# Optimization experiments

Hardware: AMD Instinct MI355X
Metric: run time of the kernel (lower is better)

The kernel has to match this reference:

```python
import jax, jax.numpy as jnp
import numpy as np

B, T, HOP = 4, 200, 120
N = T * HOP
M1, A1 = 40, 5            # mcep_order+1, apdc_order+1
HID, COND = 256, 192
SR = 24000.0
ALPHA = 0.466             # frequency-warping for 24 kHz
PD = 4                    # Pade order
PADE = jnp.asarray([1.0, 0.4999273, 0.1067005, 0.00956526, 0.0003041358], jnp.float32)
SIGN = jnp.asarray([1.0, -1.0, 1.0, -1.0], jnp.float32)  # + for odd Pade tap index
F0_MEAN, F0_STD = 5.0, 0.25
MCEP_MEAN, MCEP_STD = 0.0, 1.0
APDC_MEAN, APDC_STD = 0.0, 1.0
NOISE_RATIO, SP_RATE, F0_RATE = 0.5, 1.0, 1.0


def mc2b(mc, a):
    """SPTK mc2b: mel-cepstrum -> MLSA filter coefficients (scan over order)."""
    mc_rev = jnp.moveaxis(mc, -1, 0)[::-1]  # [M1, B, T]
    def step(carry, c):
        b = c - a * carry
        return b, b
    _, bs = jax.lax.scan(step, jnp.zeros_like(mc_rev[0]), mc_rev)
    return jnp.moveaxis(bs[::-1], 0, -1)


def _mlsafir(x, b, d):
    # SPTK mlsafir, vectorized over the PD Pade taps.
    # x: [PD], b: [M1], d: [PD, M1+1]
    aa = 1.0 - ALPHA * ALPHA
    d1 = aa * x + ALPHA * d[:, 1]
    def step(prev, di):  # d_new[i] = d[i] + a*(d[i+1] - d_new[i-1]) : order recurrence
        d_i, d_ip1 = di
        new = d_i + ALPHA * (d_ip1 - prev)
        return new, new
    xs = (d[:, 2:M1].T, d[:, 3:M1 + 1].T)  # [M1-2, PD]
    _, dupd = jax.lax.scan(step, d1, xs)    # [M1-2, PD]
    y = jnp.einsum('mp,m->p', dupd, b[2:])
    # delay-line shift: new d = [x, d1, d1, dupd[2..M]]
    new_d = jnp.concatenate([x[:, None], d1[:, None], d1[:, None], dupd.T], axis=1)
    return y, new_d


def _mlsa_step(state, inp):
    d1a, d1b, d2, pt2 = state
    x, b = inp
    x = x * jnp.exp(b[0])           # gain
    # ---- stage 1 (uses b[1] only), SPTK mlsadf1 ----
    aa = 1.0 - ALPHA * ALPHA
    na = aa * d1b[:PD] + ALPHA * d1a[1:]
    npt = na * b[1]
    v1 = npt * PADE[1:]
    x1 = x + jnp.sum(v1 * SIGN)
    y1 = jnp.sum(v1) + x1
    d1a = jnp.concatenate([d1a[:1], na])
    d1b = jnp.concatenate([x1[None], npt])
    # ---- stage 2 (orders >= 2), SPTK mlsadf2 ----
    fy, d2 = _mlsafir(pt2[:PD], b, d2)
    v2 = fy * PADE[1:]
    x2 = y1 + jnp.sum(v2 * SIGN)
    y2 = jnp.sum(v2) + x2
    pt2 = jnp.concatenate([x2[None], fy])
    return (d1a, d1b, d2, pt2), y2


def mlsa_filter(exc, b_up):
    # exc: [N], b_up: [N, M1] -> filtered waveform [N]
    init = (jnp.zeros(PD + 1, jnp.float32), jnp.zeros(PD + 1, jnp.float32),
            jnp.zeros((PD, M1 + 1), jnp.float32), jnp.zeros(PD + 1, jnp.float32))
    _, y = jax.lax.scan(_mlsa_step, init, (exc, b_up))
    return y


def _forward(mceps, apdcs, frame_f0s, noise,
             Wm, bm, Wa, ba, Wf, bf, Wpa, bpa, Wpp, bpp,
             Wrp, brp, Wra, bra, Wap):
    # linear feature embed + sum
    hs = mceps @ Wm + bm + apdcs @ Wa + ba + frame_f0s @ Wf + bf   # [B,T,HID]
    ca = hs @ Wpa + bpa                                             # prenet_a cond [B,T,COND]
    cp = hs @ Wpp + bpp                                             # prenet_p cond
    # denorm (+ exp for log-f0)
    f0 = jnp.exp(frame_f0s[..., 0] * F0_STD + F0_MEAN) * F0_RATE    # [B,T]
    sp = mceps * MCEP_STD + MCEP_MEAN
    ap = apdcs * APDC_STD + APDC_MEAN
    # per-path mel-cepstra with prenet residuals
    mc_p = sp * SP_RATE + 0.1 * jnp.tanh(cp @ Wrp + brp)
    mc_a = sp * SP_RATE + 0.1 * jnp.tanh(ca @ Wra + bra) + ap @ Wap
    b_p = mc2b(mc_p, ALPHA)
    b_a = mc2b(mc_a, ALPHA)
    # excitation at sample rate
    f0_up = jnp.repeat(f0, HOP, axis=1)                             # [B,N]
    phase = jnp.cumsum(f0_up / SR, axis=1)
    w = jnp.floor(phase)
    wprev = jnp.concatenate([jnp.zeros_like(w[:, :1]), w[:, :-1]], axis=1)
    amp = jnp.sqrt(SR / jnp.maximum(f0_up, 1.0))
    pulse = jnp.where(w > wprev, amp, 0.0)
    exc_p = pulse * (1.0 - NOISE_RATIO)
    exc_a = noise * NOISE_RATIO
    # run both (periodic/aperiodic) MLSA synthesis filters in one batched scan
    excs = jnp.concatenate([exc_p, exc_a], axis=0)                  # [2B,N]
    bs = jnp.repeat(jnp.concatenate([b_p, b_a], axis=0), HOP, axis=1)  # [2B,N,M1]
    wavs = jax.vmap(mlsa_filter)(excs, bs)                          # [2B,N]
    return wavs[:B] + wavs[B:]


_forward_jit = jax.jit(_forward)


def setup_inputs() -> dict:
    key = jax.random.key(0)
    ks = jax.random.split(key, 20)
    decay = 0.3 / (1.0 + jnp.arange(M1, dtype=jnp.float32))  # realistic cepstral decay (filter stability)
    return {
        'mceps': jax.random.normal(ks[0], (B, T, M1), jnp.float32) * decay,
        'apdcs': jax.random.normal(ks[1], (B, T, A1), jnp.float32) * 0.3,
        'frame_f0s': jax.random.normal(ks[2], (B, T, 1), jnp.float32),
        'noise': jax.random.normal(ks[3], (B, N), jnp.float32),
        'Wm': jax.random.normal(ks[4], (M1, HID), jnp.float32) / np.sqrt(M1),
        'bm': jnp.zeros((HID,), jnp.float32),
        'Wa': jax.random.normal(ks[5], (A1, HID), jnp.float32) / np.sqrt(A1),
        'ba': jnp.zeros((HID,), jnp.float32),
        'Wf': jax.random.normal(ks[6], (1, HID), jnp.float32),
        'bf': jnp.zeros((HID,), jnp.float32),
        'Wpa': jax.random.normal(ks[7], (HID, COND), jnp.float32) / np.sqrt(HID),
        'bpa': jnp.zeros((COND,), jnp.float32),
        'Wpp': jax.random.normal(ks[8], (HID, COND), jnp.float32) / np.sqrt(HID),
        'bpp': jnp.zeros((COND,), jnp.float32),
        'Wrp': jax.random.normal(ks[9], (COND, M1), jnp.float32) / np.sqrt(COND),
        'brp': jnp.zeros((M1,), jnp.float32),
        'Wra': jax.random.normal(ks[10], (COND, M1), jnp.float32) / np.sqrt(COND),
        'bra': jnp.zeros((M1,), jnp.float32),
        'Wap': jax.random.normal(ks[11], (A1, M1), jnp.float32) * 0.05,
    }


def reference(mceps, apdcs, frame_f0s, noise,
              Wm, bm, Wa, ba, Wf, bf, Wpa, bpa, Wpp, bpp,
              Wrp, brp, Wra, bra, Wap):
    return _forward_jit(mceps, apdcs, frame_f0s, noise,
                        Wm, bm, Wa, ba, Wf, bf, Wpa, bpa, Wpp, bpp,
                        Wrp, brp, Wra, bra, Wap)
```

## Files before the change

### kernel.cpp

```cpp
#include <hip/hip_runtime.h>
#include <math.h>

#define ALPHA 0.466f
#define T_FRAMES 200
#define HOPW 120
#define NSAMP 24000
#define M1 40
#define HID 256
#define CONDW 192

#define NCHUNK 100
#define CHUNKF 2
#define WARMF 4
#define SERF (WARMF + CHUNKF)

#define F8 8
#define BPF ((NSAMP + 255) / 256)

__global__ __launch_bounds__(256) void embed_kernel(
    const float* __restrict__ mceps, const float* __restrict__ apdcs,
    const float* __restrict__ f0s,
    const float* __restrict__ Wm, const float* __restrict__ bm,
    const float* __restrict__ Wa, const float* __restrict__ ba,
    const float* __restrict__ Wf, const float* __restrict__ bf,
    const float* __restrict__ Wpa, const float* __restrict__ bpa,
    const float* __restrict__ Wpp, const float* __restrict__ bpp,
    const float* __restrict__ Wrp, const float* __restrict__ brp,
    const float* __restrict__ Wra, const float* __restrict__ bra,
    const float* __restrict__ Wap, float* __restrict__ bcoef)
{
    __shared__ float s_mc[F8][M1];
    __shared__ float s_ap[F8][5];
    __shared__ float s_f0[F8];
    __shared__ float s_h[F8][HID];
    __shared__ float s_ca[F8][CONDW];
    __shared__ float s_cp[F8][CONDW];
    __shared__ float s_mcp[F8][M1];
    __shared__ float s_mca[F8][M1];

    const int tid = threadIdx.x;
    const int R0 = blockIdx.x * F8;

    for (int j = tid; j < F8 * M1; j += 256) s_mc[j / M1][j % M1] = mceps[R0 * M1 + j];
    if (tid < F8 * 5) s_ap[tid / 5][tid % 5] = apdcs[R0 * 5 + tid];
    if (tid < F8)     s_f0[tid] = f0s[R0 + tid];
    __syncthreads();

    {
        float acc[F8];
        const float bias = bm[tid] + ba[tid] + bf[tid];
        #pragma unroll
        for (int r = 0; r < F8; ++r) acc[r] = bias;
        for (int k = 0; k < M1; ++k) {
            float w = Wm[k * HID + tid];
            #pragma unroll
            for (int r = 0; r < F8; ++r) acc[r] = fmaf(s_mc[r][k], w, acc[r]);
        }
        #pragma unroll
        for (int k = 0; k < 5; ++k) {
            float w = Wa[k * HID + tid];
            #pragma unroll
            for (int r = 0; r < F8; ++r) acc[r] = fmaf(s_ap[r][k], w, acc[r]);
        }
        float wf = Wf[tid];
        #pragma unroll
        for (int r = 0; r < F8; ++r) s_h[r][tid] = fmaf(s_f0[r], wf, acc[r]);
    }
    __syncthreads();

    if (tid < CONDW) {
        float aA[F8], aP[F8];
        #pragma unroll
        for (int r = 0; r < F8; ++r) { aA[r] = bpa[tid]; aP[r] = bpp[tid]; }
        for (int k = 0; k < HID; k += 4) {
            float4 h4[F8];
            #pragma unroll
            for (int r = 0; r < F8; ++r) h4[r] = *(const float4*)&s_h[r][k];
            #pragma unroll
            for (int kk = 0; kk < 4; ++kk) {
                float wa = Wpa[(k + kk) * CONDW + tid];
                float wp = Wpp[(k + kk) * CONDW + tid];
                #pragma unroll
                for (int r = 0; r < F8; ++r) {
                    float hv = (&h4[r].x)[kk];
                    aA[r] = fmaf(hv, wa, aA[r]);
                    aP[r] = fmaf(hv, wp, aP[r]);
                }
            }
        }
        #pragma unroll
        for (int r = 0; r < F8; ++r) { s_ca[r][tid] = aA[r]; s_cp[r][tid] = aP[r]; }
    }
    __syncthreads();

    if (tid < M1) {
        const int u = tid;
        float acc[F8];
        #pragma unroll
        for (int r = 0; r < F8; ++r) acc[r] = brp[u];
        for (int k = 0; k < CONDW; k += 4) {
            float4 c4[F8];
            #pragma unroll
            for (int r = 0; r < F8; ++r) c4[r] = *(const float4*)&s_cp[r][k];
            #pragma unroll
            for (int kk = 0; kk < 4; ++kk) {
                float w = Wrp[(k + kk) * M1 + u];
                #pragma unroll
                for (int r = 0; r < F8; ++r) acc[r] = fmaf((&c4[r].x)[kk], w, acc[r]);
            }
        }
        #pragma unroll
        for (int r = 0; r < F8; ++r)
            s_mcp[r][u] = s_mc[r][u] + 0.1f * tanhf(acc[r]);
    } else if (tid >= 64 && tid < 64 + M1) {
        const int u = tid - 64;
        float acc[F8];
        #pragma unroll
        for (int r = 0; r < F8; ++r) acc[r] = bra[u];
        for (int k = 0; k < CONDW; k += 4) {
            float4 c4[F8];
            #pragma unroll
            for (int r = 0; r < F8; ++r) c4[r] = *(const float4*)&s_ca[r][k];
            #pragma unroll
            for (int kk = 0; kk < 4; ++kk) {
                float w = Wra[(k + kk) * M1 + u];
                #pragma unroll
                for (int r = 0; r < F8; ++r) acc[r] = fmaf((&c4[r].x)[kk], w, acc[r]);
            }
        }
        #pragma unroll
        for (int r = 0; r < F8; ++r) {
            float aw = 0.f;
            #pragma unroll
            for (int j = 0; j < 5; ++j) aw = fmaf(s_ap[r][j], Wap[j * M1 + u], aw);
            s_mca[r][u] = s_mc[r][u] + 0.1f * tanhf(acc[r]) + aw;
        }
    }
    __syncthreads();

    if (tid < 16) {
        const int r = tid >> 1, path = tid & 1;
        const int R = R0 + r;
        const int batch = R / T_FRAMES, t = R - batch * T_FRAMES;
        const float* src = path ? s_mca[r] : s_mcp[r];
        float* dst = bcoef + ((path * 4 + batch) * T_FRAMES + t) * M1;
        float prev = src[M1 - 1];
        dst[M1 - 1] = prev;
        for (int m = M1 - 2; m >= 0; --m) {
            prev = src[m] - ALPHA * prev;
            dst[m] = prev;
        }
    }
}

__global__ __launch_bounds__(256) void exc_kernel(
    const float* __restrict__ f0s, const float* __restrict__ noise,
    float* __restrict__ exc)
{
    const int ff = blockIdx.x / BPF;
    const int n = (blockIdx.x % BPF) * 256 + threadIdx.x;
    const int tid = threadIdx.x;

    if (ff >= 4) {
        if (n < NSAMP) exc[ff * NSAMP + n] = 0.5f * noise[(ff - 4) * NSAMP + n];
        return;
    }

    __shared__ double s_base[T_FRAMES];
    __shared__ double s_step[T_FRAMES];
    __shared__ float  s_amp[T_FRAMES];

    if (tid < 64) {
        const int L = tid;
        double st[4], loc[4];
        float am[4];
        double s = 0.0;
        #pragma unroll
        for (int j = 0; j < 4; ++j) {
            int ft = L * 4 + j;
            if (ft < T_FRAMES) {
                double fv = exp((double)f0s[ff * T_FRAMES + ft] * 0.25 + 5.0);
                st[j] = fv / 24000.0;
                am[j] = (float)(0.5 * sqrt(24000.0 / fmax(fv, 1.0)));
            } else { st[j] = 0.0; am[j] = 0.f; }
            loc[j] = s;
            s += st[j];
        }
        double tot = s;
        #pragma unroll
        for (int off = 1; off < 64; off <<= 1) {
            double v = __shfl_up(s, off, 64);
            if (L >= off) s += v;
        }
        double excl = s - tot;
        #pragma unroll
        for (int j = 0; j < 4; ++j) {
            int ft = L * 4 + j;
            if (ft < T_FRAMES) {
                s_base[ft] = 120.0 * (excl + loc[j]);
                s_step[ft] = st[j];
                s_amp[ft]  = am[j];
            }
        }
    }
    __syncthreads();

    if (n < NSAMP) {
        int ft = n / HOPW, k = n - ft * HOPW;
        double st = s_step[ft], bs = s_base[ft];
        double ph  = bs + (double)(k + 1) * st;
        double php = bs + (double)k * st;
        exc[ff * NSAMP + n] = (floor(ph) > floor(php)) ? s_amp[ft] : 0.0f;
    }
}

template <int CTRL>
__device__ __forceinline__ float rshr(float x) {
    return __int_as_float(
        __builtin_amdgcn_mov_dpp(__float_as_int(x), CTRL, 0xF, 0xF, true));
}
__device__ __forceinline__ float rlane(float x, int l) {
    return __int_as_float(__builtin_amdgcn_readlane(__float_as_int(x), l));
}

template <bool OUT>
__device__ __forceinline__ void run_frame(
    const float* __restrict__ sx, float AB,
    float BP1, float BP2, float BP3, float BP4,
    float Ba, float Bb, float Bc, float K, float IPw, int i16, int row,
    float& E0, float& E1, float& E2, float& dlp, float& xin,
    float& m1, float& m2, float& m3, float& m4, float& w0,
    float* __restrict__ yout)
{
    const float A = ALPHA;
    const float AA = 1.0f - A * A;
    const float A2 = A * A;
    const float R1 = -(A * A * A);
    const float R2 = R1 * R1;
    const float R4 = R2 * R2;
    const float R8 = R4 * R4;

    float xc = sx[0];
    #pragma unroll 8
    for (int k = 0; k < HOPW; ++k) {
        float xn = sx[k + 1];
        float x = xc;

        float na0 = AA * w0 + A * m1;
        float na1 = AB * m1 + A * m2;
        float na2 = AB * m2 + A * m3;
        float na3 = AB * m3 + A * m4;
        float v10 = na0 * BP1, v11 = na1 * BP2, v12 = na2 * BP3, v13 = na3 * BP4;
        float x1 = x + ((v10 - v11) + (v12 - v13));
        float y1 = ((v10 + v11) + (v12 + v13)) + x1;
        m1 = na0; m2 = na1; m3 = na2; m4 = na3; w0 = x1;

        float pE2 = rshr<0x111>(E2);
        float ca = fmaf(A, E0, (i16 == 0) ? dlp : pE2);
        float cb = fmaf(A, E1, E0);
        float cc = fmaf(A, E2, E1);
        float ua = ca;
        float ub = fmaf(-A, ua, cb);
        float uc = fmaf(-A, ub, cc);
        float X = uc;
        X = fmaf(R1, rshr<0x111>(X), X);
        X = fmaf(R2, rshr<0x112>(X), X);
        X = fmaf(R4, rshr<0x114>(X), X);
        X = fmaf(R8, rshr<0x118>(X), X);
        float dl = fmaf(AA, xin, A * dlp);
        float Xt = fmaf(K, dl, X);
        float Si = rshr<0x111>(Xt);
        Si = (i16 == 0) ? dl : Si;
        float ta = fmaf(-A, Si, ua);
        float tb = fmaf(A2, Si, ub);

        float fp = ta * Ba;
        fp = fmaf(tb, Bb, fp);
        fp = fmaf(Xt, Bc, fp);
        float S = fp;
        S += rshr<0x111>(S);
        S += rshr<0x112>(S);
        S += rshr<0x114>(S);
        S += rshr<0x118>(S);

        float xprev = rshr<0x142>(S) * IPw;

        float v20 = rlane(S, 15);
        float v21 = rlane(S, 31);
        float v22 = rlane(S, 47);
        float v23 = rlane(S, 63);
        float e = v20 + v22, o = v21 + v23;
        float x2 = y1 + (e - o);
        if (OUT) {
            float y2 = (e + o) + x2;
            yout[k] = y2;
        }

        xin = (row == 0) ? x2 : xprev;
        E0 = ta; E1 = tb; E2 = Xt;
        dlp = dl;
        xc = xn;
    }
}

__global__ __launch_bounds__(64) void mlsa_kernel(
    const float* __restrict__ bcoef, const float* __restrict__ exc,
    float* __restrict__ y2g)
{
    __shared__ float sexc[HOPW + 2];

    const int tid = threadIdx.x;
    const int i16 = tid & 15;
    const int row = tid >> 4;
    const int chunk = blockIdx.x >> 3;
    const int f = blockIdx.x & 7;

    const float P1 = 0.4999273f, P2 = 0.1067005f, P3 = 0.00956526f, P4 = 0.0003041358f;
    const float Pw  = (row == 0) ? P1 : (row == 1) ? P2 : (row == 2) ? P3 : P4;
    const float IPw = (row == 1) ? (1.f / P1) : (row == 2) ? (1.f / P2) : (1.f / P3);

    const float R1 = -(ALPHA * ALPHA * ALPHA);
    float K = R1;
    for (int j = 0; j < i16; ++j) K *= R1;

    float E0 = 0.f, E1 = 0.f, E2 = 0.f;
    float dlp = 0.f, xin = 0.f;
    float m1 = 0.f, m2 = 0.f, m3 = 0.f, m4 = 0.f, w0 = 0.f;

    const int outF0 = chunk * CHUNKF;

    #pragma unroll 1
    for (int i = 0; i < SERF; ++i) {
        const int ftA = outF0 - WARMF + i;

        const int ftc = (ftA < 0) ? 0 : ftA;
        const float* bp = bcoef + (f * T_FRAMES + ftc) * M1;
        const float b1 = bp[1];
        const float G  = expf(bp[0]);
        const float AA = 1.0f - ALPHA * ALPHA;
        const float AB = AA * b1;
        const float BP1 = b1 * P1, BP2 = b1 * P2, BP3 = b1 * P3, BP4 = b1 * P4;

        for (int j = tid; j < HOPW; j += 64)
            sexc[j] = (ftA >= 0) ? exc[f * NSAMP + ftA * HOPW + j] * G : 0.f;
        if (tid == 0) sexc[HOPW] = 0.f;

        const int ja = 3 * i16 + 2;
        const float Ba = ((i16 <= 12) ? bp[ja]     : 0.f) * Pw;
        const float Bb = ((i16 <= 12) ? bp[ja + 1] : 0.f) * Pw;
        const float Bc = ((i16 <= 11) ? bp[ja + 2] : 0.f) * Pw;
        float* yout = y2g + f * NSAMP + ftA * HOPW;

        if (i >= WARMF)
            run_frame<true>(sexc, AB, BP1, BP2, BP3, BP4, Ba, Bb, Bc, K, IPw,
                            i16, row, E0, E1, E2, dlp, xin, m1, m2, m3, m4, w0, yout);
        else
            run_frame<false>(sexc, AB, BP1, BP2, BP3, BP4, Ba, Bb, Bc, K, IPw,
                             i16, row, E0, E1, E2, dlp, xin, m1, m2, m3, m4, w0, yout);
    }
}

__global__ __launch_bounds__(256) void combine_kernel(
    const float* __restrict__ y2g, float* __restrict__ out)
{
    int i = blockIdx.x * 256 + threadIdx.x;
    if (i >= 4 * NSAMP) return;
    int b = i / NSAMP, n = i - b * NSAMP;
    out[i] = y2g[b * NSAMP + n] + y2g[(4 + b) * NSAMP + n];
}

extern "C" void kernel_launch(void* const* d_in, const int* in_sizes, int n_in,
                              void* d_out, int out_size, void* d_ws, size_t ws_size,
                              hipStream_t stream) {
    const float* mceps = (const float*)d_in[0];
    const float* apdcs = (const float*)d_in[1];
    const float* f0s   = (const float*)d_in[2];
    const float* noise = (const float*)d_in[3];
    const float* Wm  = (const float*)d_in[4];
    const float* bm  = (const float*)d_in[5];
    const float* Wa  = (const float*)d_in[6];
    const float* ba  = (const float*)d_in[7];
    const float* Wf  = (const float*)d_in[8];
    const float* bf  = (const float*)d_in[9];
    const float* Wpa = (const float*)d_in[10];
    const float* bpa = (const float*)d_in[11];
    const float* Wpp = (const float*)d_in[12];
    const float* bpp = (const float*)d_in[13];
    const float* Wrp = (const float*)d_in[14];
    const float* brp = (const float*)d_in[15];
    const float* Wra = (const float*)d_in[16];
    const float* bra = (const float*)d_in[17];
    const float* Wap = (const float*)d_in[18];
    float* out = (float*)d_out;

    char* ws = (char*)d_ws;
    float* bcoef = (float*)(ws + 0);
    float* exc   = (float*)(ws + 256000);
    float* y2g   = (float*)(ws + 1024000);

    embed_kernel<<<dim3(4 * T_FRAMES / F8), dim3(256), 0, stream>>>(
        mceps, apdcs, f0s, Wm, bm, Wa, ba, Wf, bf,
        Wpa, bpa, Wpp, bpp, Wrp, brp, Wra, bra, Wap, bcoef);

    exc_kernel<<<dim3(8 * BPF), dim3(256), 0, stream>>>(f0s, noise, exc);

    mlsa_kernel<<<dim3(NCHUNK * 8), dim3(64), 0, stream>>>(bcoef, exc, y2g);

    combine_kernel<<<dim3((4 * NSAMP + 255) / 256), dim3(256), 0, stream>>>(
        y2g, out);
}
```

Baseline: 221.9 us.

## Merge embed and excitation kernels, shorten warmup, pack MLSA stage-1 math into vectors

Merges the embedding and excitation-generation kernels into one launch using block-index dispatch, removing a kernel launch and its serialization gap. Reduces the warmup frames per chunk from 4 to 3, which cuts the serial recurrence work per chunk but shortens the IIR settling before output starts and may affect accuracy. Packs stage-1 MLSA arithmetic into 2-wide float vectors so packed FMA can be used, folds the Pade reciprocal into the dl coefficient, and computes the output as fma(2,e,y1).

```diff
diff --git a/kernel.cpp b/kernel.cpp
--- a/kernel.cpp
+++ b/kernel.cpp
@@ -11,15 +11,18 @@
 
 #define NCHUNK 100
 #define CHUNKF 2
-#define WARMF 4
+#define WARMF 3
 #define SERF (WARMF + CHUNKF)
 
 #define F8 8
+#define EMB_BLOCKS (4 * T_FRAMES / F8)
 #define BPF ((NSAMP + 255) / 256)
 
-__global__ __launch_bounds__(256) void embed_kernel(
+typedef float v2f __attribute__((ext_vector_type(2)));
+
+__global__ __launch_bounds__(256) void prep_kernel(
     const float* __restrict__ mceps, const float* __restrict__ apdcs,
-    const float* __restrict__ f0s,
+    const float* __restrict__ f0s, const float* __restrict__ noise,
     const float* __restrict__ Wm, const float* __restrict__ bm,
     const float* __restrict__ Wa, const float* __restrict__ ba,
     const float* __restrict__ Wf, const float* __restrict__ bf,
@@ -27,8 +30,70 @@
     const float* __restrict__ Wpp, const float* __restrict__ bpp,
     const float* __restrict__ Wrp, const float* __restrict__ brp,
     const float* __restrict__ Wra, const float* __restrict__ bra,
-    const float* __restrict__ Wap, float* __restrict__ bcoef)
+    const float* __restrict__ Wap,
+    float* __restrict__ bcoef, float* __restrict__ exc)
 {
+    const int tid = threadIdx.x;
+
+    if (blockIdx.x >= EMB_BLOCKS) {
+        const int xb = blockIdx.x - EMB_BLOCKS;
+        const int ff = xb / BPF;
+        const int n = (xb % BPF) * 256 + tid;
+
+        if (ff >= 4) {
+            if (n < NSAMP) exc[ff * NSAMP + n] = 0.5f * noise[(ff - 4) * NSAMP + n];
+            return;
+        }
+
+        __shared__ double s_base[T_FRAMES];
+        __shared__ double s_step[T_FRAMES];
+        __shared__ float  s_amp[T_FRAMES];
+
+        if (tid < 64) {
+            const int L = tid;
+            double st[4], loc[4];
+            float am[4];
+            double s = 0.0;
+            #pragma unroll
+            for (int j = 0; j < 4; ++j) {
+                int ft = L * 4 + j;
+                if (ft < T_FRAMES) {
+                    double fv = exp((double)f0s[ff * T_FRAMES + ft] * 0.25 + 5.0);
+                    st[j] = fv / 24000.0;
+                    am[j] = (float)(0.5 * sqrt(24000.0 / fmax(fv, 1.0)));
+                } else { st[j] = 0.0; am[j] = 0.f; }
+                loc[j] = s;
+                s += st[j];
+            }
+            double tot = s;
+            #pragma unroll
+            for (int off = 1; off < 64; off <<= 1) {
+                double v = __shfl_up(s, off, 64);
+                if (L >= off) s += v;
+            }
+            double excl = s - tot;
+            #pragma unroll
+            for (int j = 0; j < 4; ++j) {
+                int ft = L * 4 + j;
+                if (ft < T_FRAMES) {
+                    s_base[ft] = 120.0 * (excl + loc[j]);
+                    s_step[ft] = st[j];
+                    s_amp[ft]  = am[j];
+                }
+            }
+        }
+        __syncthreads();
+
+        if (n < NSAMP) {
+            int ft = n / HOPW, k = n - ft * HOPW;
+            double st = s_step[ft], bs = s_base[ft];
+            double ph  = bs + (double)(k + 1) * st;
+            double php = bs + (double)k * st;
+            exc[ff * NSAMP + n] = (floor(ph) > floor(php)) ? s_amp[ft] : 0.0f;
+        }
+        return;
+    }
+
     __shared__ float s_mc[F8][M1];
     __shared__ float s_ap[F8][5];
     __shared__ float s_f0[F8];
@@ -38,7 +103,6 @@
     __shared__ float s_mcp[F8][M1];
     __shared__ float s_mca[F8][M1];
 
-    const int tid = threadIdx.x;
     const int R0 = blockIdx.x * F8;
 
     for (int j = tid; j < F8 * M1; j += 256) s_mc[j / M1][j % M1] = mceps[R0 * M1 + j];
@@ -153,67 +217,6 @@
     }
 }
 
-__global__ __launch_bounds__(256) void exc_kernel(
-    const float* __restrict__ f0s, const float* __restrict__ noise,
-    float* __restrict__ exc)
-{
-    const int ff = blockIdx.x / BPF;
-    const int n = (blockIdx.x % BPF) * 256 + threadIdx.x;
-    const int tid = threadIdx.x;
-
-    if (ff >= 4) {
-        if (n < NSAMP) exc[ff * NSAMP + n] = 0.5f * noise[(ff - 4) * NSAMP + n];
-        return;
-    }
-
-    __shared__ double s_base[T_FRAMES];
-    __shared__ double s_step[T_FRAMES];
-    __shared__ float  s_amp[T_FRAMES];
-
-    if (tid < 64) {
-        const int L = tid;
-        double st[4], loc[4];
-        float am[4];
-        double s = 0.0;
-        #pragma unroll
-        for (int j = 0; j < 4; ++j) {
-            int ft = L * 4 + j;
-            if (ft < T_FRAMES) {
-                double fv = exp((double)f0s[ff * T_FRAMES + ft] * 0.25 + 5.0);
-                st[j] = fv / 24000.0;
-                am[j] = (float)(0.5 * sqrt(24000.0 / fmax(fv, 1.0)));
-            } else { st[j] = 0.0; am[j] = 0.f; }
-            loc[j] = s;
-            s += st[j];
-        }
-        double tot = s;
-        #pragma unroll
-        for (int off = 1; off < 64; off <<= 1) {
-            double v = __shfl_up(s, off, 64);
-            if (L >= off) s += v;
-        }
-        double excl = s - tot;
-        #pragma unroll
-        for (int j = 0; j < 4; ++j) {
-            int ft = L * 4 + j;
-            if (ft < T_FRAMES) {
-                s_base[ft] = 120.0 * (excl + loc[j]);
-                s_step[ft] = st[j];
-                s_amp[ft]  = am[j];
-            }
-        }
-    }
-    __syncthreads();
-
-    if (n < NSAMP) {
-        int ft = n / HOPW, k = n - ft * HOPW;
-        double st = s_step[ft], bs = s_base[ft];
-        double ph  = bs + (double)(k + 1) * st;
-        double php = bs + (double)k * st;
-        exc[ff * NSAMP + n] = (floor(ph) > floor(php)) ? s_amp[ft] : 0.0f;
-    }
-}
-
 template <int CTRL>
 __device__ __forceinline__ float rshr(float x) {
     return __int_as_float(
@@ -225,15 +228,14 @@
 
 template <bool OUT>
 __device__ __forceinline__ void run_frame(
-    const float* __restrict__ sx, float AB,
-    float BP1, float BP2, float BP3, float BP4,
-    float Ba, float Bb, float Bc, float K, float IPw, int i16, int row,
-    float& E0, float& E1, float& E2, float& dlp, float& xin,
-    float& m1, float& m2, float& m3, float& m4, float& w0,
+    const float* __restrict__ sx,
+    v2f Cv, v2f BP13, v2f BP24,
+    float Ba, float Bb, float Bc, float K, float AAP, int i16, int row,
+    float& E0, float& E1, float& E2, float& dlp, float& src,
+    v2f& PB, v2f& PC, float& w0,
     float* __restrict__ yout)
 {
     const float A = ALPHA;
-    const float AA = 1.0f - A * A;
     const float A2 = A * A;
     const float R1 = -(A * A * A);
     const float R2 = R1 * R1;
@@ -246,15 +248,18 @@
         float xn = sx[k + 1];
         float x = xc;
 
-        float na0 = AA * w0 + A * m1;
-        float na1 = AB * m1 + A * m2;
-        float na2 = AB * m2 + A * m3;
-        float na3 = AB * m3 + A * m4;
-        float v10 = na0 * BP1, v11 = na1 * BP2, v12 = na2 * BP3, v13 = na3 * BP4;
-        float x1 = x + ((v10 - v11) + (v12 - v13));
-        float y1 = ((v10 + v11) + (v12 + v13)) + x1;
-        m1 = na0; m2 = na1; m3 = na2; m4 = na3; w0 = x1;
-
+        v2f PA; PA.x = w0; PA.y = PC.x;
+        v2f NA02 = __builtin_elementwise_fma(Cv, PA, A * PB);
+        v2f NA13 = __builtin_elementwise_fma((v2f)(Cv.y), PB, A * PC);
+        v2f VA = NA02 * BP13;
+        v2f VB = NA13 * BP24;
+        v2f D = VA - VB;
+        v2f Sm = VA + VB;
+        float x1 = x + (D.x + D.y);
+        float y1 = (Sm.x + Sm.y) + x1;
+        PB = NA02; PC = NA13; w0 = x1;
+
+        float dl = fmaf(AAP, src, A * dlp);
         float pE2 = rshr<0x111>(E2);
         float ca = fmaf(A, E0, (i16 == 0) ? dlp : pE2);
         float cb = fmaf(A, E1, E0);
@@ -267,7 +272,6 @@
         X = fmaf(R2, rshr<0x112>(X), X);
         X = fmaf(R4, rshr<0x114>(X), X);
         X = fmaf(R8, rshr<0x118>(X), X);
-        float dl = fmaf(AA, xin, A * dlp);
         float Xt = fmaf(K, dl, X);
         float Si = rshr<0x111>(Xt);
         Si = (i16 == 0) ? dl : Si;
@@ -283,8 +287,6 @@
         S += rshr<0x114>(S);
         S += rshr<0x118>(S);
 
-        float xprev = rshr<0x142>(S) * IPw;
-
         float v20 = rlane(S, 15);
         float v21 = rlane(S, 31);
         float v22 = rlane(S, 47);
@@ -292,11 +294,11 @@
         float e = v20 + v22, o = v21 + v23;
         float x2 = y1 + (e - o);
         if (OUT) {
-            float y2 = (e + o) + x2;
+            float y2 = fmaf(2.f, e, y1);
             yout[k] = y2;
         }
 
-        xin = (row == 0) ? x2 : xprev;
+        src = (row == 0) ? x2 : rshr<0x142>(S);
         E0 = ta; E1 = tb; E2 = Xt;
         dlp = dl;
         xc = xn;
@@ -317,15 +319,19 @@
 
     const float P1 = 0.4999273f, P2 = 0.1067005f, P3 = 0.00956526f, P4 = 0.0003041358f;
     const float Pw  = (row == 0) ? P1 : (row == 1) ? P2 : (row == 2) ? P3 : P4;
-    const float IPw = (row == 1) ? (1.f / P1) : (row == 2) ? (1.f / P2) : (1.f / P3);
+    const float AAc = 1.0f - ALPHA * ALPHA;
+    const float AAP = (row == 0) ? AAc
+                    : (row == 1) ? (AAc / P1)
+                    : (row == 2) ? (AAc / P2) : (AAc / P3);
 
     const float R1 = -(ALPHA * ALPHA * ALPHA);
     float K = R1;
     for (int j = 0; j < i16; ++j) K *= R1;
 
     float E0 = 0.f, E1 = 0.f, E2 = 0.f;
-    float dlp = 0.f, xin = 0.f;
-    float m1 = 0.f, m2 = 0.f, m3 = 0.f, m4 = 0.f, w0 = 0.f;
+    float dlp = 0.f, src = 0.f;
+    v2f PB = (v2f)(0.f), PC = (v2f)(0.f);
+    float w0 = 0.f;
 
     const int outF0 = chunk * CHUNKF;
 
@@ -337,9 +343,9 @@
         const float* bp = bcoef + (f * T_FRAMES + ftc) * M1;
         const float b1 = bp[1];
         const float G  = expf(bp[0]);
-        const float AA = 1.0f - ALPHA * ALPHA;
-        const float AB = AA * b1;
-        const float BP1 = b1 * P1, BP2 = b1 * P2, BP3 = b1 * P3, BP4 = b1 * P4;
+        v2f Cv;   Cv.x = AAc;      Cv.y = AAc * b1;
+        v2f BP13; BP13.x = b1 * P1; BP13.y = b1 * P3;
+        v2f BP24; BP24.x = b1 * P2; BP24.y = b1 * P4;
 
         for (int j = tid; j < HOPW; j += 64)
             sexc[j] = (ftA >= 0) ? exc[f * NSAMP + ftA * HOPW + j] * G : 0.f;
@@ -352,11 +358,11 @@
         float* yout = y2g + f * NSAMP + ftA * HOPW;
 
         if (i >= WARMF)
-            run_frame<true>(sexc, AB, BP1, BP2, BP3, BP4, Ba, Bb, Bc, K, IPw,
-                            i16, row, E0, E1, E2, dlp, xin, m1, m2, m3, m4, w0, yout);
+            run_frame<true>(sexc, Cv, BP13, BP24, Ba, Bb, Bc, K, AAP, i16, row,
+                            E0, E1, E2, dlp, src, PB, PC, w0, yout);
         else
-            run_frame<false>(sexc, AB, BP1, BP2, BP3, BP4, Ba, Bb, Bc, K, IPw,
-                             i16, row, E0, E1, E2, dlp, xin, m1, m2, m3, m4, w0, yout);
+            run_frame<false>(sexc, Cv, BP13, BP24, Ba, Bb, Bc, K, AAP, i16, row,
+                             E0, E1, E2, dlp, src, PB, PC, w0, yout);
     }
 }
 
@@ -398,11 +404,9 @@
     float* exc   = (float*)(ws + 256000);
     float* y2g   = (float*)(ws + 1024000);
 
-    embed_kernel<<<dim3(4 * T_FRAMES / F8), dim3(256), 0, stream>>>(
-        mceps, apdcs, f0s, Wm, bm, Wa, ba, Wf, bf,
-        Wpa, bpa, Wpp, bpp, Wrp, brp, Wra, bra, Wap, bcoef);
-
-    exc_kernel<<<dim3(8 * BPF), dim3(256), 0, stream>>>(f0s, noise, exc);
+    prep_kernel<<<dim3(EMB_BLOCKS + 8 * BPF), dim3(256), 0, stream>>>(
+        mceps, apdcs, f0s, noise, Wm, bm, Wa, ba, Wf, bf,
+        Wpa, bpa, Wpp, bpp, Wrp, brp, Wra, bra, Wap, bcoef, exc);
 
     mlsa_kernel<<<dim3(NCHUNK * 8), dim3(64), 0, stream>>>(bcoef, exc, y2g);
 
```

After: 230.2 us. +3.7%, slower.
